# Optimization experiments

Measured on AMD Instinct MI355X. Metric: run time of the kernel, lower is better.

## Reference

```python
import jax, jax.numpy as jnp
import numpy as np

MARGIN = 0.2


def setup_inputs() -> dict:
    key = jax.random.key(0)
    k1, k2 = jax.random.split(key)
    N, D, C = 512, 256, 64
    embeddings = jax.random.normal(k1, (N, D), dtype=jnp.float32)
    labels = jax.random.randint(k2, (N,), 0, C, dtype=jnp.int64)
    return {"embeddings": embeddings, "labels": labels}


def reference(embeddings, labels):
    # Faithful vectorization of the python-loop semi-hard triplet mining.
    # The original iterates unordered positive pairs (i<j) and treats BOTH i and j
    # as anchors, i.e. all ordered positive pairs (a, p), a != p, labels[a]==labels[p].
    # For each such pair it picks a uniformly-random negative n with
    #   pd[a,n] > pd[a,p]  and  pd[a,n]^2 < pd[a,p]^2 + margin,
    # and the loss only uses SQUARED distances, so we work with sqd directly
    # (all comparisons are monotone in the square for non-negative distances).
    n = embeddings.shape[0]
    sq_norm = jnp.sum(embeddings * embeddings, axis=-1)  # [N]
    # squared pairwise distances (== torch.cdist(...)**2), clamped for fp error
    sqd = jnp.maximum(sq_norm[:, None] + sq_norm[None, :]
                      - 2.0 * (embeddings @ embeddings.T), 0.0)  # [N, N]

    same = labels[:, None] == labels[None, :]                     # [N, N]
    pos_pair = same & ~jnp.eye(n, dtype=bool)                     # ordered positive pairs (a, p)

    # valid[a, p, j]: j is an admissible negative for anchor a w.r.t. positive p
    d_ap = sqd[:, :, None]        # sqd[a, p] broadcast over j
    d_aj = sqd[:, None, :]        # sqd[a, j] broadcast over p
    valid = (~same)[:, None, :] & (d_aj > d_ap) & (d_aj < d_ap + MARGIN)  # [N, N, N]
    has_neg = jnp.any(valid, axis=-1)                             # [N, N]

    # uniform random choice among valid negatives via Gumbel-argmax
    gumbel = jax.random.gumbel(jax.random.key(42), (n, n, n), dtype=jnp.float32)
    scores = jnp.where(valid, gumbel, -jnp.inf)
    j_star = jnp.argmax(scores, axis=-1)                          # [N, N]
    d_an_sq = jnp.take_along_axis(sqd, j_star, axis=1)            # sqd[a, j_star[a, p]]

    contrib = (pos_pair & has_neg).astype(sqd.dtype)              # [N, N]
    terms = sqd - d_an_sq + MARGIN                                # d_ap^2 - d_an^2 + margin
    count = jnp.maximum(jnp.sum(contrib), 1.0)
    loss = jnp.sum(terms * contrib) / count
    return loss
```

## Files before the change

kernel.cpp:

```cpp
#include <hip/hip_runtime.h>
#include <cstdint>

#define NPTS 512
#define DIM 256
#define NBLK (NPTS / 2)
#define TK 32
#define LDSW 132
#define MARGIN_F 0.2f
#define FIX_SCALE 1073741824.0
#define SUM_BITS 42
#define CNT_SHIFT 42
#define DONE_SHIFT 56

__device__ __forceinline__ uint32_t rotl32(uint32_t x, uint32_t r) {
  return (x << r) | (x >> (32u - r));
}

__device__ __forceinline__ uint32_t threefry_bits(uint32_t c1) {
  const uint32_t k0 = 0u, k1 = 42u;
  const uint32_t k2 = k0 ^ k1 ^ 0x1BD11BDAu;
  uint32_t x0 = 0u + k0;
  uint32_t x1 = c1 + k1;
#define TFR(r) { x0 += x1; x1 = rotl32(x1, r); x1 ^= x0; }
  TFR(13u) TFR(15u) TFR(26u) TFR(6u)
  x0 += k1; x1 += k2 + 1u;
  TFR(17u) TFR(29u) TFR(16u) TFR(24u)
  x0 += k2; x1 += k0 + 2u;
  TFR(13u) TFR(15u) TFR(26u) TFR(6u)
  x0 += k0; x1 += k1 + 3u;
  TFR(17u) TFR(29u) TFR(16u) TFR(24u)
  x0 += k1; x1 += k2 + 4u;
  TFR(13u) TFR(15u) TFR(26u) TFR(6u)
  x0 += k2; x1 += k0 + 5u;
#undef TFR
  return x0 ^ x1;
}

__global__ __launch_bounds__(512) void gram_kernel(
    const float* __restrict__ emb,
    float* __restrict__ G,
    float* __restrict__ dg,
    unsigned long long* __restrict__ gsum)
{
  __shared__ float As[TK][LDSW];
  __shared__ float Bs[TK][LDSW];

  const int b = blockIdx.x;
  const int ti = b >> 4, tj = b & 15;
  const int t = threadIdx.x;
  const int ty = t >> 4;
  const int tx = t & 15;

  if (b == 0 && t == 0) *gsum = 0ull;

  float acc0 = 0.f, acc1 = 0.f;
  #pragma unroll
  for (int kh = 0; kh < 2; ++kh) {
    const int koff = kh << 7;
    __syncthreads();
    #pragma unroll
    for (int q = 0; q < 2; ++q) {
      const int f = t * 2 + q;
      const int r = f >> 5;
      const int c4 = f & 31;
      const float4 va = *reinterpret_cast<const float4*>(emb + (ti * TK + r) * DIM + koff + c4 * 4);
      const float4 vb = *reinterpret_cast<const float4*>(emb + (tj * TK + r) * DIM + koff + c4 * 4);
      *reinterpret_cast<float4*>(&As[r][c4 * 4]) = va;
      *reinterpret_cast<float4*>(&Bs[r][c4 * 4]) = vb;
    }
    __syncthreads();
    #pragma unroll 8
    for (int k4 = 0; k4 < 32; ++k4) {
      const float4 a  = *reinterpret_cast<const float4*>(&As[ty][k4 * 4]);
      const float4 b0 = *reinterpret_cast<const float4*>(&Bs[tx][k4 * 4]);
      const float4 b1 = *reinterpret_cast<const float4*>(&Bs[tx + 16][k4 * 4]);
      acc0 += a.x * b0.x + a.y * b0.y + a.z * b0.z + a.w * b0.w;
      acc1 += a.x * b1.x + a.y * b1.y + a.z * b1.z + a.w * b1.w;
    }
  }
  const int gr = ti * TK + ty;
  const int gc0 = tj * TK + tx;
  G[gr * NPTS + gc0]      = acc0;
  G[gr * NPTS + gc0 + 16] = acc1;
  if (ti == tj) {
    if (ty == tx)           dg[gr] = acc0;
    else if (ty == tx + 16) dg[gr] = acc1;
  }
}

__global__ __launch_bounds__(512) void semihard_kernel(
    const float* __restrict__ G,
    const float* __restrict__ dg,
    const int* __restrict__ labels,
    unsigned long long* __restrict__ gsum,
    float* __restrict__ out)
{
  __shared__ float sd0[NPTS];
  __shared__ float sd1[NPTS];
  __shared__ int   slab[NPTS];
  __shared__ int   plist[256];
  __shared__ int   pcnt;
  __shared__ unsigned long long wsum[8], wcnt[8];

  const int a0 = blockIdx.x * 2;
  const int a1 = a0 + 1;
  const int t = threadIdx.x;
  const int wave = t >> 6;
  const int lane = t & 63;

  if (t == 0) pcnt = 0;

  {
    const float da0 = dg[a0];
    const float da1 = dg[a1];
    const float dt  = dg[t];
    const float g0 = G[a0 * NPTS + t];
    const float g1 = G[a1 * NPTS + t];
    slab[t] = labels[t];
    const float v0 = da0 + dt - 2.f * g0;
    const float v1 = da1 + dt - 2.f * g1;
    sd0[t] = v0 > 0.f ? v0 : 0.f;
    sd1[t] = v1 > 0.f ? v1 : 0.f;
  }
  __syncthreads();

  {
    const int lp = slab[t];
    if (t != a0 && lp == slab[a0]) { int k = atomicAdd(&pcnt, 1); plist[k] = t; }
    if (t != a1 && lp == slab[a1]) { int k = atomicAdd(&pcnt, 1); plist[k] = (1 << 16) | t; }
  }
  __syncthreads();

  unsigned long long lsum = 0ull, lcnt = 0ull;
  const int np = pcnt;
  for (int e = wave; e < np; e += 8) {
    const int ent = plist[e];
    const int ai = ent >> 16;
    const int p = ent & 0xffff;
    const float* drp = ai ? sd1 : sd0;
    const int ag = ai ? a1 : a0;
    const int la = slab[ag];
    const float dap = drp[p];
    const float hi = dap + MARGIN_F;
    const uint32_t base = ((uint32_t)ag << 18) | ((uint32_t)p << 9);

    int bestKey = -1, bestJ = 0;
    #pragma unroll
    for (int k = 0; k < 8; ++k) {
      const int j = lane + (k << 6);
      const float dj = drp[j];
      if (slab[j] != la && dj > dap && dj < hi) {
        const int key = (int)(threefry_bits(base + (uint32_t)j) >> 9);
        if (key > bestKey) { bestKey = key; bestJ = j; }
      }
    }
    #pragma unroll
    for (int m = 32; m; m >>= 1) {
      const int ok = __shfl_xor(bestKey, m);
      const int oj = __shfl_xor(bestJ, m);
      if (ok > bestKey || (ok == bestKey && oj < bestJ)) { bestKey = ok; bestJ = oj; }
    }
    if (lane == 0 && bestKey >= 0) {
      const float term = (dap - drp[bestJ]) + MARGIN_F;
      lsum += (unsigned long long)((double)term * FIX_SCALE + 0.5);
      lcnt += 1ull;
    }
  }

  if (lane == 0) { wsum[wave] = lsum; wcnt[wave] = lcnt; }
  __syncthreads();
  if (t == 0) {
    unsigned long long s = 0ull, c = 0ull;
    #pragma unroll
    for (int w = 0; w < 8; ++w) { s += wsum[w]; c += wcnt[w]; }
    const unsigned long long contrib =
        (1ull << DONE_SHIFT) | (c << CNT_SHIFT) | s;
    const unsigned long long old = atomicAdd(gsum, contrib);
    if ((old >> DONE_SHIFT) == (unsigned long long)(NBLK - 1)) {
      const unsigned long long tot = old + contrib;
      const unsigned long long sum = tot & ((1ull << SUM_BITS) - 1ull);
      const unsigned long long cnt = (tot >> CNT_SHIFT) & 0x3FFFull;
      const double sd = (double)sum / FIX_SCALE;
      const double cd = cnt ? (double)cnt : 1.0;
      out[0] = (float)(sd / cd);
    }
  }
}

extern "C" void kernel_launch(void* const* d_in, const int* in_sizes, int n_in,
                              void* d_out, int out_size, void* d_ws, size_t ws_size,
                              hipStream_t stream) {
  const float* emb  = (const float*)d_in[0];
  const int* labels = (const int*)d_in[1];
  float* out        = (float*)d_out;

  float* G  = (float*)d_ws;
  float* dg = (float*)((char*)d_ws + NPTS * NPTS * 4);
  unsigned long long* gsum =
      (unsigned long long*)((char*)d_ws + NPTS * NPTS * 4 + 2048);

  gram_kernel<<<dim3(256), dim3(512), 0, stream>>>(emb, G, dg, gsum);
  semihard_kernel<<<dim3(NBLK), dim3(512), 0, stream>>>(G, dg, labels, gsum, out);
}
```

Measured before the change: 18.75 us.

## Compute Gram matrix with split-bf16 MFMA instead of scalar FP32 dot products

The Gram kernel now converts each embedding tile to bf16 hi/lo pairs in shared memory and computes the dot products with 16x16x32 bf16 MFMA instructions. Three MFMAs per step (hi*hi, hi*lo, lo*hi) approximate FP32 accuracy. The whole K dimension is staged at once, and only 4 of the 8 waves do matrix work. The workspace layout is also reordered. The lo*lo term is dropped, so small rounding differences could change which semi-hard negatives pass the threshold tests.

Result: faster. 17.17 us (-8.4%).

```diff
diff --git a/kernel.cpp b/kernel.cpp
--- a/kernel.cpp
+++ b/kernel.cpp
@@ -5,15 +5,26 @@
 #define DIM 256
 #define NBLK (NPTS / 2)
 #define TK 32
-#define LDSW 132
+#define LDB 264
 #define MARGIN_F 0.2f
 #define FIX_SCALE 1073741824.0
 #define SUM_BITS 42
 #define CNT_SHIFT 42
 #define DONE_SHIFT 56
 
+typedef __attribute__((ext_vector_type(8))) short bf16x8;
+typedef __attribute__((ext_vector_type(4))) float f32x4;
+
 __device__ __forceinline__ uint32_t rotl32(uint32_t x, uint32_t r) {
   return (x << r) | (x >> (32u - r));
+}
+
+__device__ __forceinline__ ushort f2bf(float f) {
+  uint32_t u = __float_as_uint(f);
+  return (ushort)((u + 0x7FFFu + ((u >> 16) & 1u)) >> 16);
+}
+__device__ __forceinline__ float bf2f(ushort h) {
+  return __uint_as_float(((uint32_t)h) << 16);
 }
 
 __device__ __forceinline__ uint32_t threefry_bits(uint32_t c1) {
@@ -42,49 +53,68 @@
     float* __restrict__ dg,
     unsigned long long* __restrict__ gsum)
 {
-  __shared__ float As[TK][LDSW];
-  __shared__ float Bs[TK][LDSW];
+  __shared__ __align__(16) ushort Ahi[TK][LDB];
+  __shared__ __align__(16) ushort Alo[TK][LDB];
+  __shared__ __align__(16) ushort Bhi[TK][LDB];
+  __shared__ __align__(16) ushort Blo[TK][LDB];
 
   const int b = blockIdx.x;
   const int ti = b >> 4, tj = b & 15;
   const int t = threadIdx.x;
-  const int ty = t >> 4;
-  const int tx = t & 15;
+  const int wave = t >> 6;
+  const int lane = t & 63;
 
   if (b == 0 && t == 0) *gsum = 0ull;
 
-  float acc0 = 0.f, acc1 = 0.f;
   #pragma unroll
-  for (int kh = 0; kh < 2; ++kh) {
-    const int koff = kh << 7;
-    __syncthreads();
-    #pragma unroll
-    for (int q = 0; q < 2; ++q) {
-      const int f = t * 2 + q;
-      const int r = f >> 5;
-      const int c4 = f & 31;
-      const float4 va = *reinterpret_cast<const float4*>(emb + (ti * TK + r) * DIM + koff + c4 * 4);
-      const float4 vb = *reinterpret_cast<const float4*>(emb + (tj * TK + r) * DIM + koff + c4 * 4);
-      *reinterpret_cast<float4*>(&As[r][c4 * 4]) = va;
-      *reinterpret_cast<float4*>(&Bs[r][c4 * 4]) = vb;
-    }
-    __syncthreads();
-    #pragma unroll 8
-    for (int k4 = 0; k4 < 32; ++k4) {
-      const float4 a  = *reinterpret_cast<const float4*>(&As[ty][k4 * 4]);
-      const float4 b0 = *reinterpret_cast<const float4*>(&Bs[tx][k4 * 4]);
-      const float4 b1 = *reinterpret_cast<const float4*>(&Bs[tx + 16][k4 * 4]);
-      acc0 += a.x * b0.x + a.y * b0.y + a.z * b0.z + a.w * b0.w;
-      acc1 += a.x * b1.x + a.y * b1.y + a.z * b1.z + a.w * b1.w;
-    }
-  }
-  const int gr = ti * TK + ty;
-  const int gc0 = tj * TK + tx;
-  G[gr * NPTS + gc0]      = acc0;
-  G[gr * NPTS + gc0 + 16] = acc1;
-  if (ti == tj) {
-    if (ty == tx)           dg[gr] = acc0;
-    else if (ty == tx + 16) dg[gr] = acc1;
+  for (int q = 0; q < 4; ++q) {
+    const int idx = (q << 9) + t;
+    const int r = idx >> 6;
+    const int c4 = idx & 63;
+    const float4 va = *reinterpret_cast<const float4*>(emb + (ti * TK + r) * DIM + c4 * 4);
+    const float4 vb = (ti == tj) ? va
+        : *reinterpret_cast<const float4*>(emb + (tj * TK + r) * DIM + c4 * 4);
+    const float af[4] = {va.x, va.y, va.z, va.w};
+    const float bf[4] = {vb.x, vb.y, vb.z, vb.w};
+    #pragma unroll
+    for (int e = 0; e < 4; ++e) {
+      const int c = c4 * 4 + e;
+      const ushort ah = f2bf(af[e]);
+      Ahi[r][c] = ah;
+      Alo[r][c] = f2bf(af[e] - bf2f(ah));
+      const ushort bh = f2bf(bf[e]);
+      Bhi[r][c] = bh;
+      Blo[r][c] = f2bf(bf[e] - bf2f(bh));
+    }
+  }
+  __syncthreads();
+
+  if (wave < 4) {
+    const int qr = wave >> 1, qc = wave & 1;
+    const int frow = qr * 16 + (lane & 15);
+    const int fcol = qc * 16 + (lane & 15);
+    const int kg = lane >> 4;
+
+    f32x4 acc = {0.f, 0.f, 0.f, 0.f};
+    #pragma unroll
+    for (int s = 0; s < 8; ++s) {
+      const int kb = s * 32 + kg * 8;
+      const bf16x8 ah = *reinterpret_cast<const bf16x8*>(&Ahi[frow][kb]);
+      const bf16x8 al = *reinterpret_cast<const bf16x8*>(&Alo[frow][kb]);
+      const bf16x8 bh = *reinterpret_cast<const bf16x8*>(&Bhi[fcol][kb]);
+      const bf16x8 bl = *reinterpret_cast<const bf16x8*>(&Blo[fcol][kb]);
+      acc = __builtin_amdgcn_mfma_f32_16x16x32_bf16(ah, bh, acc, 0, 0, 0);
+      acc = __builtin_amdgcn_mfma_f32_16x16x32_bf16(ah, bl, acc, 0, 0, 0);
+      acc = __builtin_amdgcn_mfma_f32_16x16x32_bf16(al, bh, acc, 0, 0, 0);
+    }
+
+    const int lc = qc * 16 + (lane & 15);
+    #pragma unroll
+    for (int j = 0; j < 4; ++j) {
+      const int lr = qr * 16 + (lane >> 4) * 4 + j;
+      G[(ti * TK + lr) * NPTS + (tj * TK + lc)] = acc[j];
+      if (ti == tj && lr == lc) dg[ti * TK + lr] = acc[j];
+    }
   }
 }
 
@@ -194,10 +224,10 @@
   const int* labels = (const int*)d_in[1];
   float* out        = (float*)d_out;
 
-  float* G  = (float*)d_ws;
-  float* dg = (float*)((char*)d_ws + NPTS * NPTS * 4);
-  unsigned long long* gsum =
-      (unsigned long long*)((char*)d_ws + NPTS * NPTS * 4 + 2048);
+  char* ws = (char*)d_ws;
+  unsigned long long* gsum = (unsigned long long*)ws;
+  float* dg = (float*)(ws + 2048);
+  float* G  = (float*)(ws + 8192);
 
   gram_kernel<<<dim3(256), dim3(512), 0, stream>>>(emb, G, dg, gsum);
   semihard_kernel<<<dim3(NBLK), dim3(512), 0, stream>>>(G, dg, labels, gsum, out);
```
